# Performance work log

Hardware: AMD Instinct MI355X
Metric: run time of the kernel (lower is better)

The kernel has to match this reference:

```python
import jax, jax.numpy as jnp
import numpy as np

B, S, HID = 2, 2048, 1024
H, KV, D = 8, 4, 128
GROUPS = H // KV
SCALE = D ** -0.5
ROPE_THETA = 10000.0


def _rope_tables(seq_len, dim):
    inv = 1.0 / (ROPE_THETA ** (jnp.arange(0, dim, 2, dtype=jnp.float32) / dim))
    t = jnp.arange(seq_len, dtype=jnp.float32)
    freqs = jnp.outer(t, inv)                          # [S, D/2]
    emb = jnp.concatenate([freqs, freqs], axis=-1)     # [S, D]
    return jnp.cos(emb), jnp.sin(emb)


def _rotate_half(x):
    x1, x2 = jnp.split(x, 2, axis=-1)
    return jnp.concatenate([-x2, x1], axis=-1)


def setup_inputs() -> dict:
    key = jax.random.key(0)
    ks = jax.random.split(key, 7)
    std = 0.02
    hidden = jax.random.normal(ks[0], (B, S, HID), jnp.float32)
    Wq = jax.random.normal(ks[1], (HID, H * D), jnp.float32) * std
    Wk = jax.random.normal(ks[2], (HID, KV * D), jnp.float32) * std
    Wv = jax.random.normal(ks[3], (HID, KV * D), jnp.float32) * std
    Wdt = jax.random.normal(ks[4], (KV * D, H), jnp.float32) * std
    A = jax.random.normal(ks[5], (H,), jnp.float32) * 0.1
    Wo = jax.random.normal(ks[6], (H * D, HID), jnp.float32) * std
    cos, sin = _rope_tables(S, D)
    causal_mask = jnp.triu(jnp.ones((S, S), jnp.int32), 1)[None, None]  # 1 = masked
    return dict(hidden=hidden, Wq=Wq, Wk=Wk, Wv=Wv, Wdt=Wdt, A=A, Wo=Wo,
                cos=cos, sin=sin, causal_mask=causal_mask)


def reference(hidden, Wq, Wk, Wv, Wdt, A, Wo, cos, sin, causal_mask):
    # q/k/v projections -> [B, heads, S, D]
    q = (hidden @ Wq).reshape(B, S, H, D).transpose(0, 2, 1, 3)
    k = (hidden @ Wk).reshape(B, S, KV, D).transpose(0, 2, 1, 3)
    v = (hidden @ Wv).reshape(B, S, KV, D).transpose(0, 2, 1, 3)
    # RoPE
    c = cos[None, None]  # [1,1,S,D]
    s = sin[None, None]
    q = q * c + _rotate_half(q) * s
    k = k * c + _rotate_half(k) * s
    # dynamic mask: dt_proj over flattened per-position value states
    v_flat = v.transpose(0, 2, 1, 3).reshape(B, S, KV * D)
    dt = v_flat @ Wdt                                        # [B, S, H]
    dyn = jnp.exp(A[None, None, :] * jax.nn.softplus(dt))    # [B, S, H]
    attn_bias = dyn.transpose(0, 2, 1)[:, :, None, :]        # [B, H, 1, kv]
    min_val = jnp.finfo(jnp.float32).min
    attn_bias = jnp.where(causal_mask != 0, min_val, attn_bias)  # [B, H, S, S]
    # GQA repeat of kv heads
    k_rep = jnp.repeat(k, GROUPS, axis=1)
    v_rep = jnp.repeat(v, GROUPS, axis=1)
    scores = jnp.einsum('bhqd,bhkd->bhqk', q, k_rep) * SCALE + attn_bias
    w = jax.nn.softmax(scores.astype(jnp.float32), axis=-1).astype(hidden.dtype)
    out = jnp.einsum('bhqk,bhkd->bhqd', w, v_rep)
    out = out.transpose(0, 2, 1, 3).reshape(B, S, H * D)
    return out @ Wo
```

## Files before the change

### kernel.cpp

```cpp
#include <hip/hip_runtime.h>

typedef unsigned short u16;
typedef unsigned int   u32;
typedef __bf16 bf16;
typedef bf16  bf16x8 __attribute__((ext_vector_type(8)));
typedef float f32x4  __attribute__((ext_vector_type(4)));

#define S_LEN 2048
#define SCALE 0.08838834764831845f
#define SMAX  8.0f

__device__ __forceinline__ float bf2f(u16 u) {
  union { u32 i; float f; } v; v.i = ((u32)u) << 16; return v.f;
}
__device__ __forceinline__ u16 f2b(float f) {
  union { float f; u32 i; } v; v.f = f;
  u32 x = v.i;
  u32 r = x + 0x7fffu + ((x >> 16) & 1u);
  return (u16)(r >> 16);
}
__device__ __forceinline__ float2 bfpair(u32 u) {
  union { u32 i; float f; } lo, hi;
  lo.i = u << 16; hi.i = u & 0xffff0000u;
  float2 r; r.x = lo.f; r.y = hi.f; return r;
}

__device__ __forceinline__ void gl_lds16(const u16* g, u16* l) {
  __builtin_amdgcn_global_load_lds(
      (const __attribute__((address_space(1))) void*)g,
      (__attribute__((address_space(3))) void*)l, 16, 0, 0);
}

__device__ __forceinline__ void load16(const float* p, u16* dst) {
  #pragma unroll
  for (int i = 0; i < 16; i += 4) {
    float4 v = *(const float4*)(p + i);
    dst[i]     = f2b(v.x); dst[i + 1] = f2b(v.y);
    dst[i + 2] = f2b(v.z); dst[i + 3] = f2b(v.w);
  }
}

__device__ __forceinline__ void storeo(float* p, float v) { *p = v; }
__device__ __forceinline__ void storeo(u16* p, float v)   { *p = f2b(v); }

__device__ __forceinline__ bf16x8 frag8(const u16* p) {
  union { uint4 u; bf16x8 v; } c;
  c.u = *(const uint4*)p;
  return c.v;
}
__device__ __forceinline__ f32x4 zero4() {
  f32x4 z = {0.f, 0.f, 0.f, 0.f}; return z;
}

__global__ __launch_bounds__(256) void prep_kernel(
    const float* __restrict__ H, u16* __restrict__ HB,
    const float* __restrict__ Wq, const float* __restrict__ Wk,
    const float* __restrict__ Wv, const float* __restrict__ Wo,
    u16* __restrict__ Wqt, u16* __restrict__ Wkt,
    u16* __restrict__ Wvt, u16* __restrict__ Wot)
{
  const int bid = blockIdx.x;
  if (bid < 2048) {
    const size_t base = ((size_t)bid * 256 + threadIdx.x) * 8;
    float4 a = *(const float4*)(H + base);
    float4 b = *(const float4*)(H + base + 4);
    u16 tmp[8];
    tmp[0]=f2b(a.x); tmp[1]=f2b(a.y); tmp[2]=f2b(a.z); tmp[3]=f2b(a.w);
    tmp[4]=f2b(b.x); tmp[5]=f2b(b.y); tmp[6]=f2b(b.z); tmp[7]=f2b(b.w);
    *(uint4*)(HB + base) = *(uint4*)tmp;
    return;
  }
  const int b2 = bid - 2048;
  const float* src; u16* dst; int N, ko, no;
  if (b2 < 256)      { src = Wq; dst = Wqt; N = 1024; int q = b2;       ko = (q >> 4) * 64; no = (q & 15) * 64; }
  else if (b2 < 384) { src = Wk; dst = Wkt; N = 512;  int q = b2 - 256; ko = (q >> 3) * 64; no = (q & 7) * 64; }
  else if (b2 < 512) { src = Wv; dst = Wvt; N = 512;  int q = b2 - 384; ko = (q >> 3) * 64; no = (q & 7) * 64; }
  else               { src = Wo; dst = Wot; N = 1024; int q = b2 - 512; ko = (q >> 4) * 64; no = (q & 15) * 64; }

  __shared__ __align__(16) u16 T[64][68];
  const int t = threadIdx.x;
  const int r = t >> 2, c = (t & 3) * 16;
  {
    u16 tmp[16];
    load16(src + (size_t)(ko + r) * N + no + c, tmp);
    *(uint4*)&T[r][c]     = *(uint4*)tmp;
    *(uint4*)&T[r][c + 8] = *(uint4*)(tmp + 8);
  }
  __syncthreads();
  {
    u16 tmp[16];
    #pragma unroll
    for (int j = 0; j < 16; ++j) tmp[j] = T[c + j][r];
    u16* o = dst + (size_t)(no + r) * 1024 + ko + c;
    *(uint4*)o       = *(uint4*)tmp;
    *(uint4*)(o + 8) = *(uint4*)(tmp + 8);
  }
}

__global__ __launch_bounds__(256) void gemm3(
    const u16* __restrict__ A, int lda, int Kdim,
    const u16* __restrict__ W0, u16* __restrict__ O0, int ldo0,
    const u16* __restrict__ W1, u16* __restrict__ O1, int ldo1,
    const u16* __restrict__ W2, u16* __restrict__ O2, int ldo2,
    int c1, int c2,
    const float* __restrict__ cosb, const float* __restrict__ sinb, int ropeLim,
    u16* __restrict__ VTg)
{
  const int flat = blockIdx.y * gridDim.x + blockIdx.x;
  const int xcd = flat & 7, rr = flat >> 3;
  const int bx = ((xcd & 1) << 3) + (rr & 7);
  const int by = ((xcd >> 1) << 3) + (rr >> 3);
  const int n0 = bx * 128;
  const int m0 = by * 128;
  const u16* W; u16* O; int ldo, col;
  if (n0 < c1)      { W = W0; O = O0; ldo = ldo0; col = n0; }
  else if (n0 < c2) { W = W1; O = O1; ldo = ldo1; col = n0 - c1; }
  else              { W = W2; O = O2; ldo = ldo2; col = n0 - c2; }
  const bool doRope = (n0 < ropeLim);
  const bool isV    = (n0 >= c2);

  __shared__ __align__(16) u16 As[2][128 * 64];
  __shared__ __align__(16) u16 Bs[2][128 * 64];

  const int t    = threadIdx.x;
  const int w    = t >> 6, lane = t & 63, quad = lane >> 4, l16 = lane & 15;
  const int sw   = l16 & 7;
  const int srow = lane >> 3;
  const int schk = (lane & 7) ^ srow;
  int kcs[2];
  #pragma unroll
  for (int ks = 0; ks < 2; ++ks) kcs[ks] = ((ks * 4 + quad) ^ sw) * 8;

  const u16* Ag = A + (size_t)(m0 + w * 32 + srow) * lda + schk * 8;
  const u16* Bg = W + (size_t)(col + w * 32 + srow) * Kdim + schk * 8;

  f32x4 acc[2][8];
  #pragma unroll
  for (int i2 = 0; i2 < 2; ++i2)
    #pragma unroll
    for (int nt = 0; nt < 8; ++nt) acc[i2][nt] = zero4();

  #pragma unroll
  for (int j = 0; j < 4; ++j) {
    gl_lds16(Ag + (size_t)(j * 8) * lda, &As[0][(w * 4 + j) * 512]);
    gl_lds16(Bg + (size_t)(j * 8) * Kdim, &Bs[0][(w * 4 + j) * 512]);
  }

  int cur = 0;
  for (int k0 = 0; k0 < Kdim; k0 += 64, cur ^= 1) {
    __syncthreads();
    if (k0 + 64 < Kdim) {
      #pragma unroll
      for (int j = 0; j < 4; ++j) {
        gl_lds16(Ag + (size_t)(j * 8) * lda + k0 + 64, &As[cur ^ 1][(w * 4 + j) * 512]);
        gl_lds16(Bg + (size_t)(j * 8) * Kdim + k0 + 64, &Bs[cur ^ 1][(w * 4 + j) * 512]);
      }
    }
    #pragma unroll
    for (int ks = 0; ks < 2; ++ks) {
      bf16x8 a0 = frag8(&As[cur][(w * 32 + l16) * 64 + kcs[ks]]);
      bf16x8 a1 = frag8(&As[cur][(w * 32 + 16 + l16) * 64 + kcs[ks]]);
      #pragma unroll
      for (int nt = 0; nt < 8; ++nt) {
        bf16x8 bw = frag8(&Bs[cur][(nt * 16 + l16) * 64 + kcs[ks]]);
        acc[0][nt] = __builtin_amdgcn_mfma_f32_16x16x32_bf16(a0, bw, acc[0][nt], 0, 0, 0);
        acc[1][nt] = __builtin_amdgcn_mfma_f32_16x16x32_bf16(a1, bw, acc[1][nt], 0, 0, 0);
      }
    }
  }

  if (doRope) {
    #pragma unroll
    for (int i2 = 0; i2 < 2; ++i2)
      #pragma unroll
      for (int r = 0; r < 4; ++r) {
        const int m = m0 + w * 32 + i2 * 16 + quad * 4 + r;
        const int sp_ = m & (S_LEN - 1);
        const float* cp = cosb + (size_t)sp_ * 128;
        const float* sp = sinb + (size_t)sp_ * 128;
        #pragma unroll
        for (int nt = 0; nt < 4; ++nt) {
          const int d = nt * 16 + l16;
          const float a  = acc[i2][nt][r];
          const float bb = acc[i2][nt + 4][r];
          acc[i2][nt][r]     = a * cp[d]       - bb * sp[d];
          acc[i2][nt + 4][r] = bb * cp[d + 64] + a * sp[d + 64];
        }
      }
  }

  #pragma unroll
  for (int i2 = 0; i2 < 2; ++i2)
    #pragma unroll
    for (int nt = 0; nt < 8; ++nt)
      #pragma unroll
      for (int r = 0; r < 4; ++r) {
        const int m = m0 + w * 32 + i2 * 16 + quad * 4 + r;
        const int n = col + nt * 16 + l16;
        O[(size_t)m * ldo + n] = f2b(acc[i2][nt][r]);
      }

  if (isV) {
    #pragma unroll
    for (int i2 = 0; i2 < 2; ++i2)
      #pragma unroll
      for (int nt = 0; nt < 8; ++nt) {
        const int m = m0 + w * 32 + i2 * 16 + quad * 4;
        const int bb_ = m >> 11, ss = m & (S_LEN - 1);
        const int d = col + nt * 16 + l16;
        u16 tmp4[4];
        #pragma unroll
        for (int r = 0; r < 4; ++r) tmp4[r] = f2b(acc[i2][nt][r]);
        u16* dst = VTg + ((size_t)((bb_ * 4 + (d >> 7)) * 128 + (d & 127))) * S_LEN + ss;
        *(uint2*)dst = *(const uint2*)tmp4;
      }
  }
}

template <typename TO>
__global__ __launch_bounds__(256) void gemm2(
    const u16* __restrict__ A, int lda, int Kdim,
    const u16* __restrict__ W0, TO* __restrict__ O0, int ldo0,
    const u16* __restrict__ W1, TO* __restrict__ O1, int ldo1,
    const u16* __restrict__ W2, TO* __restrict__ O2, int ldo2,
    int c1, int c2)
{
  const int flat = blockIdx.y * gridDim.x + blockIdx.x;
  const int xcd = flat & 7, rr = flat >> 3;
  const int bx = ((xcd & 1) << 3) + (rr & 7);
  const int by = ((xcd >> 1) << 3) + (rr >> 3);
  const int n0 = bx * 64;
  const int m0 = by * 128;
  const u16* W; TO* O; int ldo, col;
  if (n0 < c1)      { W = W0; O = O0; ldo = ldo0; col = n0; }
  else if (n0 < c2) { W = W1; O = O1; ldo = ldo1; col = n0 - c1; }
  else              { W = W2; O = O2; ldo = ldo2; col = n0 - c2; }

  __shared__ __align__(16) u16 As[2][128 * 64];
  __shared__ __align__(16) u16 Bs[2][64 * 64];

  const int t    = threadIdx.x;
  const int w    = t >> 6, lane = t & 63, quad = lane >> 4, l16 = lane & 15;
  const int sw   = l16 & 7;
  const int srow = lane >> 3;
  const int schk = (lane & 7) ^ srow;
  int kcs[2];
  #pragma unroll
  for (int ks = 0; ks < 2; ++ks) kcs[ks] = ((ks * 4 + quad) ^ sw) * 8;

  const u16* Ag = A + (size_t)(m0 + w * 32 + srow) * lda + schk * 8;
  const u16* Bg = W + (size_t)(col + w * 16 + srow) * Kdim + schk * 8;

  f32x4 acc[2][4];
  #pragma unroll
  for (int i2 = 0; i2 < 2; ++i2)
    #pragma unroll
    for (int nt = 0; nt < 4; ++nt) acc[i2][nt] = zero4();

  #pragma unroll
  for (int j = 0; j < 4; ++j)
    gl_lds16(Ag + (size_t)(j * 8) * lda, &As[0][(w * 4 + j) * 512]);
  #pragma unroll
  for (int j = 0; j < 2; ++j)
    gl_lds16(Bg + (size_t)(j * 8) * Kdim, &Bs[0][(w * 2 + j) * 512]);

  int cur = 0;
  for (int k0 = 0; k0 < Kdim; k0 += 64, cur ^= 1) {
    __syncthreads();
    if (k0 + 64 < Kdim) {
      #pragma unroll
      for (int j = 0; j < 4; ++j)
        gl_lds16(Ag + (size_t)(j * 8) * lda + k0 + 64, &As[cur ^ 1][(w * 4 + j) * 512]);
      #pragma unroll
      for (int j = 0; j < 2; ++j)
        gl_lds16(Bg + (size_t)(j * 8) * Kdim + k0 + 64, &Bs[cur ^ 1][(w * 2 + j) * 512]);
    }
    #pragma unroll
    for (int ks = 0; ks < 2; ++ks) {
      bf16x8 a0 = frag8(&As[cur][(w * 32 + l16) * 64 + kcs[ks]]);
      bf16x8 a1 = frag8(&As[cur][(w * 32 + 16 + l16) * 64 + kcs[ks]]);
      #pragma unroll
      for (int nt = 0; nt < 4; ++nt) {
        bf16x8 bw = frag8(&Bs[cur][(nt * 16 + l16) * 64 + kcs[ks]]);
        acc[0][nt] = __builtin_amdgcn_mfma_f32_16x16x32_bf16(a0, bw, acc[0][nt], 0, 0, 0);
        acc[1][nt] = __builtin_amdgcn_mfma_f32_16x16x32_bf16(a1, bw, acc[1][nt], 0, 0, 0);
      }
    }
  }
  #pragma unroll
  for (int i2 = 0; i2 < 2; ++i2)
    #pragma unroll
    for (int nt = 0; nt < 4; ++nt)
      #pragma unroll
      for (int r = 0; r < 4; ++r) {
        const int m = m0 + w * 32 + i2 * 16 + quad * 4 + r;
        const int n = col + nt * 16 + l16;
        storeo(O + (size_t)m * ldo + n, acc[i2][nt][r]);
      }
}

__global__ __launch_bounds__(256) void dyn_kernel(const u16* __restrict__ Vb, const float* __restrict__ Wdt,
                                                  const float* __restrict__ Af, float* __restrict__ dynT)
{
  __shared__ __align__(16) float Wl[4096];
  const int t = threadIdx.x;
  #pragma unroll
  for (int i = 0; i < 4; ++i)
    *(float4*)&Wl[(t + i * 256) * 4] = *(const float4*)(Wdt + (t + i * 256) * 4);
  __syncthreads();

  const int wid = t >> 6, lane = t & 63;
  const int pos = blockIdx.x * 4 + wid;
  float acc[8];
  #pragma unroll
  for (int h = 0; h < 8; ++h) acc[h] = 0.f;
  for (int j = lane; j < 512; j += 64) {
    float v = bf2f(Vb[(size_t)pos * 512 + j]);
    float4 w0 = *(const float4*)&Wl[j * 8];
    float4 w1 = *(const float4*)&Wl[j * 8 + 4];
    acc[0] += v * w0.x; acc[1] += v * w0.y; acc[2] += v * w0.z; acc[3] += v * w0.w;
    acc[4] += v * w1.x; acc[5] += v * w1.y; acc[6] += v * w1.z; acc[7] += v * w1.w;
  }
  #pragma unroll
  for (int off = 32; off > 0; off >>= 1)
    #pragma unroll
    for (int h = 0; h < 8; ++h) acc[h] += __shfl_down(acc[h], off, 64);
  if (lane == 0) {
    const int b = pos >> 11, s = pos & (S_LEN - 1);
    #pragma unroll
    for (int h = 0; h < 8; ++h) {
      float dt = acc[h];
      float sp = (dt > 20.f) ? dt : log1pf(__expf(dt));
      dynT[(size_t)(b * 8 + h) * S_LEN + s] = __expf(Af[h] * sp);
    }
  }
}

__global__ __launch_bounds__(256, 2) void attn_mfma(const u16* __restrict__ Qb, const u16* __restrict__ Kb,
                                                    const u16* __restrict__ VTg, const float* __restrict__ dynT,
                                                    u16* __restrict__ ctx,
                                                    u16* __restrict__ PO, float* __restrict__ PL)
{
  const int idx = blockIdx.x;
  const int g = (idx & 7) | (((idx >> 3) & 1) << 3);
  const int b = g >> 3, h = g & 7, kvh = h >> 1;
  const int f = idx >> 4;
  int s, c, kt0, kt1;
  if (f < 16)      { s = 16 + f; c = 0; kt0 = 0; kt1 = 7; }
  else if (f < 32) { s = 47 - f; c = 1; kt0 = 8; kt1 = s >> 1; }
  else             { s = 47 - f; c = 0; kt0 = 0; kt1 = s >> 1; }
  const int q0 = s * 64;
  const int dt = s >> 1;

  __shared__ __align__(16) u16 Ks[128 * 128];
  __shared__ __align__(16) u16 Vs[128 * 128];
  __shared__ __align__(16) u16 Ps[4][16 * 128];

  const int t = threadIdx.x;
  const int wid = t >> 6, lane = t & 63, quad = lane >> 4, l16 = lane & 15;
  const int sw = l16 & 7, hi = l16 >> 3;

  int kcs[4];
  #pragma unroll
  for (int ks = 0; ks < 4; ++ks) kcs[ks] = ((ks * 4 + quad) ^ sw) * 8;

  const u16* KgL[2];
  const u16* VgL[2];
  {
    const int g0 = hi * 8 + (sw ^ quad);
    const int g1 = hi * 8 + (sw ^ quad ^ 4);
    KgL[0] = Kb + (size_t)(b * S_LEN + wid * 32 + quad) * 512 + kvh * 128 + g0 * 8;
    KgL[1] = Kb + (size_t)(b * S_LEN + wid * 32 + 4 + quad) * 512 + kvh * 128 + g1 * 8;
    VgL[0] = VTg + ((size_t)((b * 4 + kvh) * 128 + wid * 32 + quad)) * S_LEN + g0 * 8;
    VgL[1] = VTg + ((size_t)((b * 4 + kvh) * 128 + wid * 32 + 4 + quad)) * S_LEN + g1 * 8;
  }

  bf16x8 qf[4];
  {
    const u16* qrow = Qb + (size_t)(b * S_LEN + q0 + wid * 16 + l16) * 1024 + h * 128 + quad * 8;
    #pragma unroll
    for (int ks = 0; ks < 4; ++ks) qf[ks] = frag8(qrow + ks * 32);
  }

  const float* dynbase = dynT + (size_t)(b * 8 + h) * S_LEN + l16;

  f32x4 accO[8];
  #pragma unroll
  for (int nt = 0; nt < 8; ++nt) accO[nt] = zero4();
  float l_lane[4] = {0.f, 0.f, 0.f, 0.f};

  for (int kt = kt0; kt <= kt1; ++kt) {
    const int k0 = kt * 128;
    __syncthreads();
    #pragma unroll
    for (int j = 0; j < 8; ++j)
      gl_lds16(KgL[j & 1] + (size_t)(k0 + (j >> 1) * 8) * 512, &Ks[(wid * 8 + j) * 512]);
    #pragma unroll
    for (int j = 0; j < 8; ++j)
      gl_lds16(VgL[j & 1] + (size_t)((j >> 1) * 8) * S_LEN + k0, &Vs[(wid * 8 + j) * 512]);
    float dv[8];
    #pragma unroll
    for (int nt = 0; nt < 8; ++nt) dv[nt] = dynbase[k0 + nt * 16];
    __syncthreads();

    f32x4 accS[8];
    #pragma unroll
    for (int nt = 0; nt < 8; ++nt) accS[nt] = zero4();
    __builtin_amdgcn_s_setprio(1);
    #pragma unroll
    for (int ks = 0; ks < 4; ++ks)
      #pragma unroll
      for (int nt = 0; nt < 8; ++nt)
        accS[nt] = __builtin_amdgcn_mfma_f32_16x16x32_bf16(
            qf[ks], frag8(&Ks[(nt * 16 + l16) * 128 + kcs[ks]]), accS[nt], 0, 0, 0);
    __builtin_amdgcn_s_setprio(0);

    if (kt < dt) {
      #pragma unroll
      for (int nt = 0; nt < 8; ++nt)
        #pragma unroll
        for (int r = 0; r < 4; ++r) {
          float p = __expf(fmaf(accS[nt][r], SCALE, dv[nt]) - SMAX);
          l_lane[r] += p;
          const int prow = quad * 4 + r;
          Ps[wid][prow * 128 + (((nt * 2 + hi) ^ (prow & 7)) << 3) + sw] = f2b(p);
        }
    } else {
      const int qq = (s & 1) * 64 + wid * 16 + quad * 4;
      #pragma unroll
      for (int nt = 0; nt < 8; ++nt) {
        const int kk = nt * 16 + l16;
        #pragma unroll
        for (int r = 0; r < 4; ++r) {
          float p = (kk > qq + r) ? 0.f
                    : __expf(fmaf(accS[nt][r], SCALE, dv[nt]) - SMAX);
          l_lane[r] += p;
          const int prow = quad * 4 + r;
          Ps[wid][prow * 128 + (((nt * 2 + hi) ^ (prow & 7)) << 3) + sw] = f2b(p);
        }
      }
    }

    __builtin_amdgcn_s_setprio(1);
    #pragma unroll
    for (int ks = 0; ks < 4; ++ks) {
      bf16x8 a = frag8(&Ps[wid][l16 * 128 + kcs[ks]]);
      #pragma unroll
      for (int nt = 0; nt < 8; ++nt)
        accO[nt] = __builtin_amdgcn_mfma_f32_16x16x32_bf16(
            a, frag8(&Vs[(nt * 16 + l16) * 128 + kcs[ks]]), accO[nt], 0, 0, 0);
    }
    __builtin_amdgcn_s_setprio(0);
  }

  #pragma unroll
  for (int off = 1; off < 16; off <<= 1)
    #pragma unroll
    for (int r = 0; r < 4; ++r) l_lane[r] += __shfl_xor(l_lane[r], off, 64);

  if (s < 16) {
    float linv[4];
    #pragma unroll
    for (int r = 0; r < 4; ++r) linv[r] = 1.f / l_lane[r];
    #pragma unroll
    for (int nt = 0; nt < 8; ++nt)
      #pragma unroll
      for (int r = 0; r < 4; ++r) {
        const int qq = q0 + wid * 16 + quad * 4 + r;
        const int d  = nt * 16 + l16;
        ctx[(size_t)(b * S_LEN + qq) * 1024 + h * 128 + d] = f2b(accO[nt][r] * linv[r]);
      }
  } else {
    const int slot = g * 32 + (s - 16) * 2 + c;
    u16 tmp[32];
    #pragma unroll
    for (int nt = 0; nt < 8; ++nt)
      #pragma unroll
      for (int r = 0; r < 4; ++r) tmp[nt * 4 + r] = f2b(accO[nt][r]);
    u16* po = PO + (size_t)slot * 8192 + wid * 2048 + lane * 32;
    #pragma unroll
    for (int i = 0; i < 4; ++i) *(uint4*)(po + i * 8) = *(uint4*)(tmp + i * 8);
    if (l16 == 0) {
      #pragma unroll
      for (int r = 0; r < 4; ++r) PL[slot * 64 + wid * 16 + quad * 4 + r] = l_lane[r];
    }
  }
}

__global__ __launch_bounds__(256) void attn_combine(const u16* __restrict__ PO, const float* __restrict__ PL,
                                                    u16* __restrict__ ctx)
{
  const int sx = (int)blockIdx.x;
  const int s = 16 + sx;
  const int g = (int)blockIdx.y;
  const int b = g >> 3, h = g & 7;
  const int slot0 = g * 32 + sx * 2;
  const int t = threadIdx.x;
  const int wid = t >> 6, lane = t & 63, quad = lane >> 4, l16 = lane & 15;

  float acc[32];
  #pragma unroll
  for (int i = 0; i < 32; ++i) acc[i] = 0.f;
  float ls[4] = {0.f, 0.f, 0.f, 0.f};

  #pragma unroll
  for (int cth = 0; cth < 2; ++cth) {
    const u16* po = PO + (size_t)(slot0 + cth) * 8192 + wid * 2048 + lane * 32;
    #pragma unroll
    for (int i = 0; i < 4; ++i) {
      uint4 v = *(const uint4*)(po + i * 8);
      u32 u[4] = {v.x, v.y, v.z, v.w};
      #pragma unroll
      for (int j = 0; j < 4; ++j) {
        float2 p = bfpair(u[j]);
        acc[i * 8 + 2 * j]     += p.x;
        acc[i * 8 + 2 * j + 1] += p.y;
      }
    }
    #pragma unroll
    for (int r = 0; r < 4; ++r) ls[r] += PL[(slot0 + cth) * 64 + wid * 16 + quad * 4 + r];
  }

  float linv[4];
  #pragma unroll
  for (int r = 0; r < 4; ++r) linv[r] = 1.f / ls[r];
  #pragma unroll
  for (int nt = 0; nt < 8; ++nt)
    #pragma unroll
    for (int r = 0; r < 4; ++r) {
      const int qq = s * 64 + wid * 16 + quad * 4 + r;
      const int d  = nt * 16 + l16;
      ctx[(size_t)(b * S_LEN + qq) * 1024 + h * 128 + d] = f2b(acc[nt * 4 + r] * linv[r]);
    }
}

extern "C" void kernel_launch(void* const* d_in, const int* in_sizes, int n_in,
                              void* d_out, int out_size, void* d_ws, size_t ws_size,
                              hipStream_t stream)
{
  const float* hidden = (const float*)d_in[0];
  const float* Wq     = (const float*)d_in[1];
  const float* Wk     = (const float*)d_in[2];
  const float* Wv     = (const float*)d_in[3];
  const float* Wdt    = (const float*)d_in[4];
  const float* Af     = (const float*)d_in[5];
  const float* Wo     = (const float*)d_in[6];
  const float* cosb   = (const float*)d_in[7];
  const float* sinb   = (const float*)d_in[8];
  float* out = (float*)d_out;

  u16* Qb  = (u16*)d_ws;
  u16* Kb  = Qb + (size_t)4096 * 1024;
  u16* Vb  = Kb + (size_t)4096 * 512;
  u16* VTg = Vb + (size_t)4096 * 512;
  float* dynT = (float*)(VTg + (size_t)4096 * 512);
  u16* PO = (u16*)(dynT + (size_t)16 * S_LEN);
  float* PL = (float*)(PO + (size_t)16 * 32 * 8192);
  u16* HB  = (u16*)(PL + (size_t)16 * 32 * 64);
  u16* Wqt = HB  + (size_t)4096 * 1024;
  u16* Wkt = Wqt + (size_t)1024 * 1024;
  u16* Wvt = Wkt + (size_t)512 * 1024;
  u16* Wot = Wvt + (size_t)512 * 1024;
  u16* ctx = Qb;

  prep_kernel<<<2816, 256, 0, stream>>>(hidden, HB, Wq, Wk, Wv, Wo, Wqt, Wkt, Wvt, Wot);
  gemm3<<<dim3(16, 32), 256, 0, stream>>>(HB, 1024, 1024,
      Wqt, Qb, 1024,
      Wkt, Kb,  512,
      Wvt, Vb,  512,
      1024, 1536,
      cosb, sinb, 1536, VTg);
  dyn_kernel<<<1024, 256, 0, stream>>>(Vb, Wdt, Af, dynT);
  attn_mfma<<<768, 256, 0, stream>>>(Qb, Kb, VTg, dynT, ctx, PO, PL);
  attn_combine<<<dim3(16, 16), 256, 0, stream>>>(PO, PL, ctx);
  gemm2<float><<<dim3(16, 32), 256, 0, stream>>>(ctx, 1024, 1024,
      Wot, out, 1024,
      Wot, out, 1024,
      Wot, out, 1024,
      1 << 30, 1 << 30);
}
```

Measured before the change: 201.1 us.

## Double GEMM block size to 512 threads with one 16-row slab per wave

Both projection GEMM kernels now launch 8 waves per 128-row tile instead of 4, each wave owning 16 rows rather than 32. Per-wave accumulators and global-to-LDS loads are halved to match. The goal is more latency hiding and MFMA issue parallelism per CU. In exchange each B fragment read from LDS feeds only one MFMA instead of two, which raises LDS traffic per FLOP.

```diff
diff --git a/kernel.cpp b/kernel.cpp
--- a/kernel.cpp
+++ b/kernel.cpp
@@ -97,7 +97,7 @@
   }
 }
 
-__global__ __launch_bounds__(256) void gemm3(
+__global__ __launch_bounds__(512) void gemm3(
     const u16* __restrict__ A, int lda, int Kdim,
     const u16* __restrict__ W0, u16* __restrict__ O0, int ldo0,
     const u16* __restrict__ W1, u16* __restrict__ O1, int ldo1,
@@ -131,19 +131,17 @@
   #pragma unroll
   for (int ks = 0; ks < 2; ++ks) kcs[ks] = ((ks * 4 + quad) ^ sw) * 8;
 
-  const u16* Ag = A + (size_t)(m0 + w * 32 + srow) * lda + schk * 8;
-  const u16* Bg = W + (size_t)(col + w * 32 + srow) * Kdim + schk * 8;
-
-  f32x4 acc[2][8];
-  #pragma unroll
-  for (int i2 = 0; i2 < 2; ++i2)
-    #pragma unroll
-    for (int nt = 0; nt < 8; ++nt) acc[i2][nt] = zero4();
-
-  #pragma unroll
-  for (int j = 0; j < 4; ++j) {
-    gl_lds16(Ag + (size_t)(j * 8) * lda, &As[0][(w * 4 + j) * 512]);
-    gl_lds16(Bg + (size_t)(j * 8) * Kdim, &Bs[0][(w * 4 + j) * 512]);
+  const u16* Ag = A + (size_t)(m0 + w * 16 + srow) * lda + schk * 8;
+  const u16* Bg = W + (size_t)(col + w * 16 + srow) * Kdim + schk * 8;
+
+  f32x4 acc[8];
+  #pragma unroll
+  for (int nt = 0; nt < 8; ++nt) acc[nt] = zero4();
+
+  #pragma unroll
+  for (int j = 0; j < 2; ++j) {
+    gl_lds16(Ag + (size_t)(j * 8) * lda, &As[0][(w * 2 + j) * 512]);
+    gl_lds16(Bg + (size_t)(j * 8) * Kdim, &Bs[0][(w * 2 + j) * 512]);
   }
 
   int cur = 0;
@@ -151,74 +149,66 @@
     __syncthreads();
     if (k0 + 64 < Kdim) {
       #pragma unroll
-      for (int j = 0; j < 4; ++j) {
-        gl_lds16(Ag + (size_t)(j * 8) * lda + k0 + 64, &As[cur ^ 1][(w * 4 + j) * 512]);
-        gl_lds16(Bg + (size_t)(j * 8) * Kdim + k0 + 64, &Bs[cur ^ 1][(w * 4 + j) * 512]);
+      for (int j = 0; j < 2; ++j) {
+        gl_lds16(Ag + (size_t)(j * 8) * lda + k0 + 64, &As[cur ^ 1][(w * 2 + j) * 512]);
+        gl_lds16(Bg + (size_t)(j * 8) * Kdim + k0 + 64, &Bs[cur ^ 1][(w * 2 + j) * 512]);
       }
     }
     #pragma unroll
     for (int ks = 0; ks < 2; ++ks) {
-      bf16x8 a0 = frag8(&As[cur][(w * 32 + l16) * 64 + kcs[ks]]);
-      bf16x8 a1 = frag8(&As[cur][(w * 32 + 16 + l16) * 64 + kcs[ks]]);
+      bf16x8 a0 = frag8(&As[cur][(w * 16 + l16) * 64 + kcs[ks]]);
       #pragma unroll
       for (int nt = 0; nt < 8; ++nt) {
         bf16x8 bw = frag8(&Bs[cur][(nt * 16 + l16) * 64 + kcs[ks]]);
-        acc[0][nt] = __builtin_amdgcn_mfma_f32_16x16x32_bf16(a0, bw, acc[0][nt], 0, 0, 0);
-        acc[1][nt] = __builtin_amdgcn_mfma_f32_16x16x32_bf16(a1, bw, acc[1][nt], 0, 0, 0);
+        acc[nt] = __builtin_amdgcn_mfma_f32_16x16x32_bf16(a0, bw, acc[nt], 0, 0, 0);
       }
     }
   }
 
   if (doRope) {
     #pragma unroll
-    for (int i2 = 0; i2 < 2; ++i2)
-      #pragma unroll
-      for (int r = 0; r < 4; ++r) {
-        const int m = m0 + w * 32 + i2 * 16 + quad * 4 + r;
-        const int sp_ = m & (S_LEN - 1);
-        const float* cp = cosb + (size_t)sp_ * 128;
-        const float* sp = sinb + (size_t)sp_ * 128;
-        #pragma unroll
-        for (int nt = 0; nt < 4; ++nt) {
-          const int d = nt * 16 + l16;
-          const float a  = acc[i2][nt][r];
-          const float bb = acc[i2][nt + 4][r];
-          acc[i2][nt][r]     = a * cp[d]       - bb * sp[d];
-          acc[i2][nt + 4][r] = bb * cp[d + 64] + a * sp[d + 64];
-        }
-      }
-  }
-
-  #pragma unroll
-  for (int i2 = 0; i2 < 2; ++i2)
-    #pragma unroll
-    for (int nt = 0; nt < 8; ++nt)
-      #pragma unroll
-      for (int r = 0; r < 4; ++r) {
-        const int m = m0 + w * 32 + i2 * 16 + quad * 4 + r;
-        const int n = col + nt * 16 + l16;
-        O[(size_t)m * ldo + n] = f2b(acc[i2][nt][r]);
-      }
+    for (int r = 0; r < 4; ++r) {
+      const int m = m0 + w * 16 + quad * 4 + r;
+      const int sp_ = m & (S_LEN - 1);
+      const float* cp = cosb + (size_t)sp_ * 128;
+      const float* sp = sinb + (size_t)sp_ * 128;
+      #pragma unroll
+      for (int nt = 0; nt < 4; ++nt) {
+        const int d = nt * 16 + l16;
+        const float a  = acc[nt][r];
+        const float bb = acc[nt + 4][r];
+        acc[nt][r]     = a * cp[d]       - bb * sp[d];
+        acc[nt + 4][r] = bb * cp[d + 64] + a * sp[d + 64];
+      }
+    }
+  }
+
+  #pragma unroll
+  for (int nt = 0; nt < 8; ++nt)
+    #pragma unroll
+    for (int r = 0; r < 4; ++r) {
+      const int m = m0 + w * 16 + quad * 4 + r;
+      const int n = col + nt * 16 + l16;
+      O[(size_t)m * ldo + n] = f2b(acc[nt][r]);
+    }
 
   if (isV) {
     #pragma unroll
-    for (int i2 = 0; i2 < 2; ++i2)
-      #pragma unroll
-      for (int nt = 0; nt < 8; ++nt) {
-        const int m = m0 + w * 32 + i2 * 16 + quad * 4;
-        const int bb_ = m >> 11, ss = m & (S_LEN - 1);
-        const int d = col + nt * 16 + l16;
-        u16 tmp4[4];
-        #pragma unroll
-        for (int r = 0; r < 4; ++r) tmp4[r] = f2b(acc[i2][nt][r]);
-        u16* dst = VTg + ((size_t)((bb_ * 4 + (d >> 7)) * 128 + (d & 127))) * S_LEN + ss;
-        *(uint2*)dst = *(const uint2*)tmp4;
-      }
+    for (int nt = 0; nt < 8; ++nt) {
+      const int m = m0 + w * 16 + quad * 4;
+      const int bb_ = m >> 11, ss = m & (S_LEN - 1);
+      const int d = col + nt * 16 + l16;
+      u16 tmp4[4];
+      #pragma unroll
+      for (int r = 0; r < 4; ++r) tmp4[r] = f2b(acc[nt][r]);
+      u16* dst = VTg + ((size_t)((bb_ * 4 + (d >> 7)) * 128 + (d & 127))) * S_LEN + ss;
+      *(uint2*)dst = *(const uint2*)tmp4;
+    }
   }
 }
 
 template <typename TO>
-__global__ __launch_bounds__(256) void gemm2(
+__global__ __launch_bounds__(512) void gemm2(
     const u16* __restrict__ A, int lda, int Kdim,
     const u16* __restrict__ W0, TO* __restrict__ O0, int ldo0,
     const u16* __restrict__ W1, TO* __restrict__ O1, int ldo1,
@@ -248,55 +238,45 @@
   #pragma unroll
   for (int ks = 0; ks < 2; ++ks) kcs[ks] = ((ks * 4 + quad) ^ sw) * 8;
 
-  const u16* Ag = A + (size_t)(m0 + w * 32 + srow) * lda + schk * 8;
-  const u16* Bg = W + (size_t)(col + w * 16 + srow) * Kdim + schk * 8;
-
-  f32x4 acc[2][4];
-  #pragma unroll
-  for (int i2 = 0; i2 < 2; ++i2)
-    #pragma unroll
-    for (int nt = 0; nt < 4; ++nt) acc[i2][nt] = zero4();
-
-  #pragma unroll
-  for (int j = 0; j < 4; ++j)
-    gl_lds16(Ag + (size_t)(j * 8) * lda, &As[0][(w * 4 + j) * 512]);
+  const u16* Ag = A + (size_t)(m0 + w * 16 + srow) * lda + schk * 8;
+  const u16* Bg = W + (size_t)(col + w * 8 + srow) * Kdim + schk * 8;
+
+  f32x4 acc[4];
+  #pragma unroll
+  for (int nt = 0; nt < 4; ++nt) acc[nt] = zero4();
+
   #pragma unroll
   for (int j = 0; j < 2; ++j)
-    gl_lds16(Bg + (size_t)(j * 8) * Kdim, &Bs[0][(w * 2 + j) * 512]);
+    gl_lds16(Ag + (size_t)(j * 8) * lda, &As[0][(w * 2 + j) * 512]);
+  gl_lds16(Bg, &Bs[0][w * 512]);
 
   int cur = 0;
   for (int k0 = 0; k0 < Kdim; k0 += 64, cur ^= 1) {
     __syncthreads();
     if (k0 + 64 < Kdim) {
       #pragma unroll
-      for (int j = 0; j < 4; ++j)
-        gl_lds16(Ag + (size_t)(j * 8) * lda + k0 + 64, &As[cur ^ 1][(w * 4 + j) * 512]);
-      #pragma unroll
       for (int j = 0; j < 2; ++j)
-        gl_lds16(Bg + (size_t)(j * 8) * Kdim + k0 + 64, &Bs[cur ^ 1][(w * 2 + j) * 512]);
+        gl_lds16(Ag + (size_t)(j * 8) * lda + k0 + 64, &As[cur ^ 1][(w * 2 + j) * 512]);
+      gl_lds16(Bg + (size_t)k0 + 64, &Bs[cur ^ 1][w * 512]);
     }
     #pragma unroll
     for (int ks = 0; ks < 2; ++ks) {
-      bf16x8 a0 = frag8(&As[cur][(w * 32 + l16) * 64 + kcs[ks]]);
-      bf16x8 a1 = frag8(&As[cur][(w * 32 + 16 + l16) * 64 + kcs[ks]]);
+      bf16x8 a0 = frag8(&As[cur][(w * 16 + l16) * 64 + kcs[ks]]);
       #pragma unroll
       for (int nt = 0; nt < 4; ++nt) {
         bf16x8 bw = frag8(&Bs[cur][(nt * 16 + l16) * 64 + kcs[ks]]);
-        acc[0][nt] = __builtin_amdgcn_mfma_f32_16x16x32_bf16(a0, bw, acc[0][nt], 0, 0, 0);
-        acc[1][nt] = __builtin_amdgcn_mfma_f32_16x16x32_bf16(a1, bw, acc[1][nt], 0, 0, 0);
-      }
-    }
-  }
-  #pragma unroll
-  for (int i2 = 0; i2 < 2; ++i2)
-    #pragma unroll
-    for (int nt = 0; nt < 4; ++nt)
-      #pragma unroll
-      for (int r = 0; r < 4; ++r) {
-        const int m = m0 + w * 32 + i2 * 16 + quad * 4 + r;
-        const int n = col + nt * 16 + l16;
-        storeo(O + (size_t)m * ldo + n, acc[i2][nt][r]);
-      }
+        acc[nt] = __builtin_amdgcn_mfma_f32_16x16x32_bf16(a0, bw, acc[nt], 0, 0, 0);
+      }
+    }
+  }
+  #pragma unroll
+  for (int nt = 0; nt < 4; ++nt)
+    #pragma unroll
+    for (int r = 0; r < 4; ++r) {
+      const int m = m0 + w * 16 + quad * 4 + r;
+      const int n = col + nt * 16 + l16;
+      storeo(O + (size_t)m * ldo + n, acc[nt][r]);
+    }
 }
 
 __global__ __launch_bounds__(256) void dyn_kernel(const u16* __restrict__ Vb, const float* __restrict__ Wdt,
@@ -564,7 +544,7 @@
   u16* ctx = Qb;
 
   prep_kernel<<<2816, 256, 0, stream>>>(hidden, HB, Wq, Wk, Wv, Wo, Wqt, Wkt, Wvt, Wot);
-  gemm3<<<dim3(16, 32), 256, 0, stream>>>(HB, 1024, 1024,
+  gemm3<<<dim3(16, 32), 512, 0, stream>>>(HB, 1024, 1024,
       Wqt, Qb, 1024,
       Wkt, Kb,  512,
       Wvt, Vb,  512,
@@ -573,7 +553,7 @@
   dyn_kernel<<<1024, 256, 0, stream>>>(Vb, Wdt, Af, dynT);
   attn_mfma<<<768, 256, 0, stream>>>(Qb, Kb, VTg, dynT, ctx, PO, PL);
   attn_combine<<<dim3(16, 16), 256, 0, stream>>>(PO, PL, ctx);
-  gemm2<float><<<dim3(16, 32), 256, 0, stream>>>(ctx, 1024, 1024,
+  gemm2<float><<<dim3(16, 32), 512, 0, stream>>>(ctx, 1024, 1024,
       Wot, out, 1024,
       Wot, out, 1024,
       Wot, out, 1024,
```

After: 196.1 us, median of 3. 1.03x faster.
